# Performance work log

Measured on AMD Instinct MI355X. Metric: run time of the kernel, lower is better.

The kernel has to match this reference:

```python
import jax, jax.numpy as jnp
import numpy as np

EPS = 1e-5

def layer_norm(x, w, b):
    m = jnp.mean(x, axis=-1, keepdims=True)
    v = jnp.mean(jnp.square(x - m), axis=-1, keepdims=True)
    return (x - m) * jax.lax.rsqrt(v + EPS) * w + b

def time_shift(x):
    # shift sequence right by one, zero-pad first step: (B,L,D)
    return jnp.pad(x[:, :-1], ((0, 0), (1, 0), (0, 0)))

def wkv(time_decay, time_first, k, v):
    # Numerically-stable RWKV v4 WKV recurrence. k,v: (B,L,D)
    w = -jnp.exp(time_decay)  # (D,) negative decay
    u = time_first            # (D,)
    B, L, D = k.shape
    kT = jnp.swapaxes(k, 0, 1)  # (L,B,D)
    vT = jnp.swapaxes(v, 0, 1)
    a0 = jnp.zeros((B, D), k.dtype)
    b0 = jnp.zeros((B, D), k.dtype)
    p0 = jnp.full((B, D), -1e38, k.dtype)

    def step(carry, kv_t):
        a, b, p = carry
        k_t, v_t = kv_t
        ww = u + k_t
        q = jnp.maximum(p, ww)
        e1 = jnp.exp(p - q)
        e2 = jnp.exp(ww - q)
        out = (e1 * a + e2 * v_t) / (e1 * b + e2)
        ww2 = p + w
        q2 = jnp.maximum(ww2, k_t)
        e1b = jnp.exp(ww2 - q2)
        e2b = jnp.exp(k_t - q2)
        return (e1b * a + e2b * v_t, e1b * b + e2b, q2), out

    _, outs = jax.lax.scan(step, (a0, b0, p0), (kT, vT))
    return jnp.swapaxes(outs, 0, 1)  # (B,L,D)

def setup_inputs() -> dict:
    key = jax.random.key(0)
    B, L, D, D_att, D_ffn = 8, 2048, 1024, 1024, 4096
    ks = jax.random.split(key, 16)
    s = 1.0 / np.sqrt(D)
    inp = {
        "x": jax.random.normal(ks[0], (B, L, D), jnp.float32),
        "ln_att_w": jnp.ones((D,), jnp.float32),
        "ln_att_b": jnp.zeros((D,), jnp.float32),
        "ln_ffn_w": jnp.ones((D,), jnp.float32),
        "ln_ffn_b": jnp.zeros((D,), jnp.float32),
        "att_time_decay": jax.random.normal(ks[1], (D_att,), jnp.float32) * 0.5,
        "att_time_first": jax.random.normal(ks[2], (D_att,), jnp.float32) * 0.5,
        "att_mix_k": jax.random.uniform(ks[3], (D,), jnp.float32),
        "att_mix_v": jax.random.uniform(ks[4], (D,), jnp.float32),
        "att_mix_r": jax.random.uniform(ks[5], (D,), jnp.float32),
        "att_Wk": jax.random.normal(ks[6], (D_att, D), jnp.float32) * s,
        "att_Wv": jax.random.normal(ks[7], (D_att, D), jnp.float32) * s,
        "att_Wr": jax.random.normal(ks[8], (D_att, D), jnp.float32) * s,
        "att_Wo": jax.random.normal(ks[9], (D, D_att), jnp.float32) * s,
        "ffn_mix_k": jax.random.uniform(ks[10], (D,), jnp.float32),
        "ffn_mix_r": jax.random.uniform(ks[11], (D,), jnp.float32),
        "ffn_Wk": jax.random.normal(ks[12], (D_ffn, D), jnp.float32) * s,
        "ffn_Wv": jax.random.normal(ks[13], (D, D_ffn), jnp.float32) * (1.0 / np.sqrt(D_ffn)),
        "ffn_Wr": jax.random.normal(ks[14], (D, D), jnp.float32) * s,
    }
    return inp

def rwkv_block(x, ln_att_w, ln_att_b, ln_ffn_w, ln_ffn_b,
               att_time_decay, att_time_first, att_mix_k, att_mix_v, att_mix_r,
               att_Wk, att_Wv, att_Wr, att_Wo,
               ffn_mix_k, ffn_mix_r, ffn_Wk, ffn_Wv, ffn_Wr):
    # --- time-mix (WKV attention) ---
    xa = layer_norm(x, ln_att_w, ln_att_b)
    xs = time_shift(xa)
    k = jnp.einsum('bld,ad->bla', xa * att_mix_k + xs * (1.0 - att_mix_k), att_Wk)
    v = jnp.einsum('bld,ad->bla', xa * att_mix_v + xs * (1.0 - att_mix_v), att_Wv)
    r = jnp.einsum('bld,ad->bla', xa * att_mix_r + xs * (1.0 - att_mix_r), att_Wr)
    att = jnp.einsum('bla,da->bld', jax.nn.sigmoid(r) * wkv(att_time_decay, att_time_first, k, v), att_Wo)
    x = x + att
    # --- channel-mix FFN ---
    xf = layer_norm(x, ln_ffn_w, ln_ffn_b)
    xs = time_shift(xf)
    kx = xf * ffn_mix_k + xs * (1.0 - ffn_mix_k)
    rx = xf * ffn_mix_r + xs * (1.0 - ffn_mix_r)
    h = jnp.square(jax.nn.relu(jnp.einsum('bld,fd->blf', kx, ffn_Wk)))
    ffn = jax.nn.sigmoid(jnp.einsum('bld,ed->ble', rx, ffn_Wr)) * jnp.einsum('blf,df->bld', h, ffn_Wv)
    return x + ffn

def reference(x, ln_att_w, ln_att_b, ln_ffn_w, ln_ffn_b,
              att_time_decay, att_time_first, att_mix_k, att_mix_v, att_mix_r,
              att_Wk, att_Wv, att_Wr, att_Wo,
              ffn_mix_k, ffn_mix_r, ffn_Wk, ffn_Wv, ffn_Wr):
    return rwkv_block(x, ln_att_w, ln_att_b, ln_ffn_w, ln_ffn_b,
                      att_time_decay, att_time_first, att_mix_k, att_mix_v, att_mix_r,
                      att_Wk, att_Wv, att_Wr, att_Wo,
                      ffn_mix_k, ffn_mix_r, ffn_Wk, ffn_Wv, ffn_Wr)
```

## Files before the change

### kernel.cpp

```cpp
#include <hip/hip_runtime.h>
#include <stdint.h>

#define DDIM 1024
#define LSEQ 2048
#define BSZ  8
#define FDIM 4096
#define MROWS (BSZ*LSEQ)
#define NCHUNK 32
#define CLEN  (LSEQ/NCHUNK)

typedef float        f32x4  __attribute__((ext_vector_type(4)));
typedef unsigned int u32x4  __attribute__((ext_vector_type(4)));

using gas_void = const __attribute__((address_space(1))) void;
using las_void = __attribute__((address_space(3))) void;

__device__ __forceinline__ void gload16(const void* g, void* l) {
    __builtin_amdgcn_global_load_lds((gas_void*)g, (las_void*)l, 16, 0, 0);
}

__device__ __forceinline__ void mfma_bf16(f32x4& d, u32x4 a, u32x4 b) {
    asm("v_mfma_f32_16x16x32_bf16 %0, %1, %2, %0" : "+v"(d) : "v"(a), "v"(b));
}

__device__ __forceinline__ unsigned short f2bf(float f) {
    __bf16 h = (__bf16)f;
    return __builtin_bit_cast(unsigned short, h);
}

__global__ __launch_bounds__(256) void cvt_bf16(const float* __restrict__ src,
                                                __bf16* __restrict__ dst, int n4)
{
    int i = blockIdx.x * 256 + threadIdx.x;
    if (i >= n4) return;
    float4 f = ((const float4*)src)[i];
    ushort4 o;
    o.x = f2bf(f.x); o.y = f2bf(f.y); o.z = f2bf(f.z); o.w = f2bf(f.w);
    ((ushort4*)dst)[i] = o;
}

__device__ __forceinline__ void blk_reduce4(float& a, float& b, float& c, float& d) {
#pragma unroll
    for (int off = 32; off >= 1; off >>= 1) {
        a += __shfl_xor(a, off, 64);
        b += __shfl_xor(b, off, 64);
        c += __shfl_xor(c, off, 64);
        d += __shfl_xor(d, off, 64);
    }
    __shared__ float sm[4][4];
    const int tid = threadIdx.x;
    if ((tid & 63) == 0) {
        sm[tid >> 6][0] = a; sm[tid >> 6][1] = b;
        sm[tid >> 6][2] = c; sm[tid >> 6][3] = d;
    }
    __syncthreads();
    a = sm[0][0] + sm[1][0] + sm[2][0] + sm[3][0];
    b = sm[0][1] + sm[1][1] + sm[2][1] + sm[3][1];
    c = sm[0][2] + sm[1][2] + sm[2][2] + sm[3][2];
    d = sm[0][3] + sm[1][3] + sm[2][3] + sm[3][3];
}

__global__ __launch_bounds__(256) void ln_mix3(
    const float* __restrict__ xin, const float* __restrict__ lnw, const float* __restrict__ lnb,
    const float* __restrict__ mkv, const float* __restrict__ mvv, const float* __restrict__ mrv,
    __bf16* __restrict__ ok, __bf16* __restrict__ ov, __bf16* __restrict__ orr)
{
    const int row = blockIdx.x;
    const int l   = row & (LSEQ - 1);
    const int tid = threadIdx.x;
    const size_t rbase = (size_t)row * DDIM;
    const float4 cur = ((const float4*)(xin + rbase))[tid];
    float4 prv = make_float4(0.f, 0.f, 0.f, 0.f);
    if (l > 0) prv = ((const float4*)(xin + rbase - DDIM))[tid];
    float s0 = cur.x + cur.y + cur.z + cur.w;
    float q0 = cur.x*cur.x + cur.y*cur.y + cur.z*cur.z + cur.w*cur.w;
    float s1 = prv.x + prv.y + prv.z + prv.w;
    float q1 = prv.x*prv.x + prv.y*prv.y + prv.z*prv.z + prv.w*prv.w;
    blk_reduce4(s0, q0, s1, q1);
    const float inv = 1.f / (float)DDIM;
    const float m0 = s0 * inv, m1 = s1 * inv;
    const float r0 = rsqrtf(fmaxf(q0 * inv - m0*m0, 0.f) + 1e-5f);
    const float r1 = rsqrtf(fmaxf(q1 * inv - m1*m1, 0.f) + 1e-5f);
    const float4 w4 = ((const float4*)lnw)[tid];
    const float4 b4 = ((const float4*)lnb)[tid];
    const float4 k4 = ((const float4*)mkv)[tid];
    const float4 v4 = ((const float4*)mvv)[tid];
    const float4 r4 = ((const float4*)mrv)[tid];
    const float cA[4] = {cur.x, cur.y, cur.z, cur.w};
    const float pA[4] = {prv.x, prv.y, prv.z, prv.w};
    const float wA[4] = {w4.x, w4.y, w4.z, w4.w};
    const float bA[4] = {b4.x, b4.y, b4.z, b4.w};
    const float kA[4] = {k4.x, k4.y, k4.z, k4.w};
    const float vA[4] = {v4.x, v4.y, v4.z, v4.w};
    const float rA[4] = {r4.x, r4.y, r4.z, r4.w};
    ushort4 pk, pv, pr;
    unsigned short* pkp = &pk.x; unsigned short* pvp = &pv.x; unsigned short* prp = &pr.x;
#pragma unroll
    for (int j = 0; j < 4; ++j) {
        float xa = (cA[j] - m0) * r0 * wA[j] + bA[j];
        float xs = (l > 0) ? ((pA[j] - m1) * r1 * wA[j] + bA[j]) : 0.f;
        pkp[j] = f2bf(xa * kA[j] + xs * (1.f - kA[j]));
        pvp[j] = f2bf(xa * vA[j] + xs * (1.f - vA[j]));
        prp[j] = f2bf(xa * rA[j] + xs * (1.f - rA[j]));
    }
    const size_t oi = (size_t)row * (DDIM/4) + tid;
    ((ushort4*)ok)[oi]  = pk;
    ((ushort4*)ov)[oi]  = pv;
    ((ushort4*)orr)[oi] = pr;
}

__global__ __launch_bounds__(256) void ln_mix2(
    const float* __restrict__ xin, const float* __restrict__ lnw, const float* __restrict__ lnb,
    const float* __restrict__ mkv, const float* __restrict__ mrv,
    __bf16* __restrict__ ok, __bf16* __restrict__ orr)
{
    const int row = blockIdx.x;
    const int l   = row & (LSEQ - 1);
    const int tid = threadIdx.x;
    const size_t rbase = (size_t)row * DDIM;
    const float4 cur = ((const float4*)(xin + rbase))[tid];
    float4 prv = make_float4(0.f, 0.f, 0.f, 0.f);
    if (l > 0) prv = ((const float4*)(xin + rbase - DDIM))[tid];
    float s0 = cur.x + cur.y + cur.z + cur.w;
    float q0 = cur.x*cur.x + cur.y*cur.y + cur.z*cur.z + cur.w*cur.w;
    float s1 = prv.x + prv.y + prv.z + prv.w;
    float q1 = prv.x*prv.x + prv.y*prv.y + prv.z*prv.z + prv.w*prv.w;
    blk_reduce4(s0, q0, s1, q1);
    const float inv = 1.f / (float)DDIM;
    const float m0 = s0 * inv, m1 = s1 * inv;
    const float r0 = rsqrtf(fmaxf(q0 * inv - m0*m0, 0.f) + 1e-5f);
    const float r1 = rsqrtf(fmaxf(q1 * inv - m1*m1, 0.f) + 1e-5f);
    const float4 w4 = ((const float4*)lnw)[tid];
    const float4 b4 = ((const float4*)lnb)[tid];
    const float4 k4 = ((const float4*)mkv)[tid];
    const float4 r4 = ((const float4*)mrv)[tid];
    const float cA[4] = {cur.x, cur.y, cur.z, cur.w};
    const float pA[4] = {prv.x, prv.y, prv.z, prv.w};
    const float wA[4] = {w4.x, w4.y, w4.z, w4.w};
    const float bA[4] = {b4.x, b4.y, b4.z, b4.w};
    const float kA[4] = {k4.x, k4.y, k4.z, k4.w};
    const float rA[4] = {r4.x, r4.y, r4.z, r4.w};
    ushort4 pk, pr;
    unsigned short* pkp = &pk.x; unsigned short* prp = &pr.x;
#pragma unroll
    for (int j = 0; j < 4; ++j) {
        float xa = (cA[j] - m0) * r0 * wA[j] + bA[j];
        float xs = (l > 0) ? ((pA[j] - m1) * r1 * wA[j] + bA[j]) : 0.f;
        pkp[j] = f2bf(xa * kA[j] + xs * (1.f - kA[j]));
        prp[j] = f2bf(xa * rA[j] + xs * (1.f - rA[j]));
    }
    const size_t oi = (size_t)row * (DDIM/4) + tid;
    ((ushort4*)ok)[oi]  = pk;
    ((ushort4*)orr)[oi] = pr;
}

__global__ __launch_bounds__(256) void wkv_phase1(
    const __bf16* __restrict__ kin, const __bf16* __restrict__ vin,
    const float* __restrict__ td,
    float* __restrict__ sa, float* __restrict__ sb, float* __restrict__ sp)
{
    const int idx = blockIdx.x * 256 + threadIdx.x;
    const int d  = idx & (DDIM - 1);
    const int bc = idx >> 10;
    const int b  = bc & (BSZ - 1);
    const int c  = bc >> 3;
    const float w = -__expf(td[d]);
    const size_t base = ((size_t)b * LSEQ + (size_t)c * CLEN) * DDIM + d;
    float a = 0.f, bbv = 0.f, p = -1e38f;
    for (int t = 0; t < CLEN; ++t) {
        const size_t off = base + (size_t)t * DDIM;
        const float kt = (float)kin[off];
        const float vt = (float)vin[off];
        const float ww2 = p + w;
        const float q2  = fmaxf(ww2, kt);
        const float e1  = __expf(ww2 - q2);
        const float e2  = __expf(kt - q2);
        a   = e1 * a   + e2 * vt;
        bbv = e1 * bbv + e2;
        p   = q2;
    }
    sa[idx] = a; sb[idx] = bbv; sp[idx] = p;
}

__global__ __launch_bounds__(256) void wkv_phase2(
    const __bf16* __restrict__ kin, const __bf16* __restrict__ vin,
    const __bf16* __restrict__ srin,
    const float* __restrict__ td, const float* __restrict__ tf,
    const float* __restrict__ sa, const float* __restrict__ sb,
    const float* __restrict__ sp,
    __bf16* __restrict__ outp)
{
    const int idx = blockIdx.x * 256 + threadIdx.x;
    const int d  = idx & (DDIM - 1);
    const int bc = idx >> 10;
    const int b  = bc & (BSZ - 1);
    const int c  = bc >> 3;
    const float w = -__expf(td[d]);
    const float u = tf[d];
    const float nw = (float)CLEN * w;

    float a = 0.f, bbv = 0.f, p = -1e38f;
    for (int j = 0; j < c; ++j) {
        const int sidx = ((j * BSZ + b) << 10) + d;
        const float aj = sa[sidx], bj = sb[sidx], pj = sp[sidx];
        const float ps = p + nw;
        const float pn = fmaxf(ps, pj);
        const float e1 = __expf(ps - pn);
        const float e2 = __expf(pj - pn);
        a   = e1 * a   + e2 * aj;
        bbv = e1 * bbv + e2 * bj;
        p   = pn;
    }

    const size_t base = ((size_t)b * LSEQ + (size_t)c * CLEN) * DDIM + d;
    for (int t = 0; t < CLEN; ++t) {
        const size_t off = base + (size_t)t * DDIM;
        const float kt = (float)kin[off];
        const float vt = (float)vin[off];
        const float sr = (float)srin[off];
        const float ww = u + kt;
        const float q  = fmaxf(p, ww);
        const float e1 = __expf(p - q);
        const float e2 = __expf(ww - q);
        const float o  = (e1 * a + e2 * vt) / (e1 * bbv + e2);
        outp[off] = (__bf16)(sr * o);
        const float ww2 = p + w;
        const float q2  = fmaxf(ww2, kt);
        const float e1b = __expf(ww2 - q2);
        const float e2b = __expf(kt - q2);
        a   = e1b * a   + e2b * vt;
        bbv = e1b * bbv + e2b;
        p   = q2;
    }
}

template<int EPI>
__global__ __launch_bounds__(512, 2)
void gemm8(const __bf16* __restrict__ A, const __bf16* __restrict__ Bw,
           float* outF, __bf16* outH,
           const float* auxF, const __bf16* __restrict__ auxH,
           int N, int K, int gy)
{
    __shared__ __align__(16) char smem[131072];
    const int tid  = threadIdx.x;
    const int lane = tid & 63;
    const int wid  = tid >> 6;
    const int wr = wid >> 2, wc = wid & 3;

    const int nwg = gridDim.x;
    const int f = blockIdx.x;
    const int g = (f & 7) * (nwg >> 3) + (f >> 3);
    const int tx = g / gy;
    const int ty = g - tx * gy;
    const size_t row0 = (size_t)tx * 256;
    const size_t col0 = (size_t)ty * 256;

    auto stage = [&](int buf, int k0, int isB, int q) {
        const int row  = q * 128 + (tid >> 2);
        const int slot = (tid & 3) ^ ((row >> 1) & 3);
        const __bf16* gp = (isB ? Bw + (col0 + row) * (size_t)K
                                : A  + (row0 + row) * (size_t)K) + k0 + slot * 8;
        char* lp = smem + buf * 32768 + isB * 16384 + q * 8192 + wid * 1024;
        gload16(gp, lp);
    };
    auto rdA = [&](int buf, int m) -> u32x4 {
        const int row  = wr * 128 + m * 16 + (lane & 15);
        const int slot = (lane >> 4) ^ ((row >> 1) & 3);
        return *(const u32x4*)(smem + buf * 32768 + row * 64 + slot * 16);
    };
    auto rdB = [&](int buf, int n) -> u32x4 {
        const int row  = wc * 64 + n * 16 + (lane & 15);
        const int slot = (lane >> 4) ^ ((row >> 1) & 3);
        return *(const u32x4*)(smem + buf * 32768 + 16384 + row * 64 + slot * 16);
    };

    f32x4 acc[8][4] = {};
    const int ns = K / 32;

    stage(0, 0, 0, 0); stage(0, 0, 0, 1); stage(0, 0, 1, 0); stage(0, 0, 1, 1);
    stage(1, 32, 0, 0); stage(1, 32, 0, 1); stage(1, 32, 1, 0); stage(1, 32, 1, 1);

    for (int t = 0; t < ns; ++t) {
        const int cb = t & 3;
        if (t < ns - 1) asm volatile("s_waitcnt vmcnt(4)" ::: "memory");
        else            asm volatile("s_waitcnt vmcnt(0)" ::: "memory");
        __builtin_amdgcn_s_barrier();

        const int pf = t + 2;
        const int pb = pf & 3;
        const int pk = pf * 32;

        u32x4 bfr[4];
#pragma unroll
        for (int n = 0; n < 4; ++n) bfr[n] = rdB(cb, n);
        u32x4 afr[4];
#pragma unroll
        for (int m = 0; m < 4; ++m) afr[m] = rdA(cb, m);
        if (pf < ns) { stage(pb, pk, 0, 0); stage(pb, pk, 0, 1); }
        __builtin_amdgcn_s_setprio(1);
#pragma unroll
        for (int m = 0; m < 4; ++m)
#pragma unroll
            for (int n = 0; n < 4; ++n)
                mfma_bf16(acc[m][n], afr[m], bfr[n]);
        __builtin_amdgcn_s_setprio(0);
        __builtin_amdgcn_s_barrier();

#pragma unroll
        for (int m = 0; m < 4; ++m) afr[m] = rdA(cb, m + 4);
        if (pf < ns) { stage(pb, pk, 1, 0); stage(pb, pk, 1, 1); }
        __builtin_amdgcn_s_setprio(1);
#pragma unroll
        for (int m = 0; m < 4; ++m)
#pragma unroll
            for (int n = 0; n < 4; ++n)
                mfma_bf16(acc[m + 4][n], afr[m], bfr[n]);
        __builtin_amdgcn_s_setprio(0);
    }
    asm volatile("s_nop 7\n\ts_nop 7\n\ts_nop 3");

    const size_t obr = row0 + wr * 128 + ((lane >> 4) << 2);
    const size_t obc = col0 + wc * 64 + (lane & 15);
#pragma unroll
    for (int m = 0; m < 8; ++m) {
#pragma unroll
        for (int n = 0; n < 4; ++n) {
#pragma unroll
            for (int j = 0; j < 4; ++j) {
                const size_t idx = (obr + m * 16 + j) * (size_t)N + obc + n * 16;
                const float v = acc[m][n][j];
                if constexpr (EPI == 1) {
                    outH[idx] = (__bf16)(1.f / (1.f + __expf(-v)));
                } else if constexpr (EPI == 2) {
                    const float t2 = fmaxf(v, 0.f);
                    outH[idx] = (__bf16)(t2 * t2);
                } else if constexpr (EPI == 3) {
                    outF[idx] = auxF[idx] + v;
                } else if constexpr (EPI == 4) {
                    outF[idx] = auxF[idx] + (float)auxH[idx] * v;
                } else {
                    outH[idx] = (__bf16)v;
                }
            }
        }
    }
}

extern "C" void kernel_launch(void* const* d_in, const int* in_sizes, int n_in,
                              void* d_out, int out_size, void* d_ws, size_t ws_size,
                              hipStream_t stream)
{
    const float* x    = (const float*)d_in[0];
    const float* lnaw = (const float*)d_in[1];
    const float* lnab = (const float*)d_in[2];
    const float* lnfw = (const float*)d_in[3];
    const float* lnfb = (const float*)d_in[4];
    const float* tdec = (const float*)d_in[5];
    const float* tfir = (const float*)d_in[6];
    const float* amk  = (const float*)d_in[7];
    const float* amv  = (const float*)d_in[8];
    const float* amr  = (const float*)d_in[9];
    const float* aWk  = (const float*)d_in[10];
    const float* aWv  = (const float*)d_in[11];
    const float* aWr  = (const float*)d_in[12];
    const float* aWo  = (const float*)d_in[13];
    const float* fmk  = (const float*)d_in[14];
    const float* fmr  = (const float*)d_in[15];
    const float* fWk  = (const float*)d_in[16];
    const float* fWv  = (const float*)d_in[17];
    const float* fWr  = (const float*)d_in[18];
    float* out = (float*)d_out;

    char* ws = (char*)d_ws;
    const size_t MiB = 1ull << 20;
    __bf16* Wk_h  = (__bf16*)ws;
    __bf16* Wv_h  = Wk_h + (1ull << 20);
    __bf16* Wr_h  = Wk_h + (2ull << 20);
    __bf16* Wo_h  = Wk_h + (3ull << 20);
    __bf16* fWk_h = Wk_h + (4ull << 20);
    __bf16* fWv_h = Wk_h + (8ull << 20);
    __bf16* fWr_h = Wk_h + (12ull << 20);
    __bf16* xk = (__bf16*)(ws + 26 * MiB);
    __bf16* xv = (__bf16*)(ws + 58 * MiB);
    __bf16* xr = (__bf16*)(ws + 90 * MiB);
    __bf16* kb = (__bf16*)(ws + 122 * MiB);
    __bf16* vb = (__bf16*)(ws + 154 * MiB);
    __bf16* sr = (__bf16*)(ws + 186 * MiB);
    float* st_a = (float*)(ws + 218 * MiB);
    float* st_b = (float*)(ws + 219 * MiB);
    float* st_p = (float*)(ws + 220 * MiB);
    __bf16* atta = xk;
    __bf16* kx   = xv;
    __bf16* rx   = xr;
    __bf16* sb   = xk;
    __bf16* hb   = (__bf16*)(ws + 90 * MiB);

    cvt_bf16<<<1024, 256, 0, stream>>>(aWk, Wk_h,  1 << 18);
    cvt_bf16<<<1024, 256, 0, stream>>>(aWv, Wv_h,  1 << 18);
    cvt_bf16<<<1024, 256, 0, stream>>>(aWr, Wr_h,  1 << 18);
    cvt_bf16<<<1024, 256, 0, stream>>>(aWo, Wo_h,  1 << 18);
    cvt_bf16<<<4096, 256, 0, stream>>>(fWk, fWk_h, 1 << 20);
    cvt_bf16<<<4096, 256, 0, stream>>>(fWv, fWv_h, 1 << 20);
    cvt_bf16<<<1024, 256, 0, stream>>>(fWr, fWr_h, 1 << 18);

    ln_mix3<<<MROWS, 256, 0, stream>>>(x, lnaw, lnab, amk, amv, amr, xk, xv, xr);

    const int gD = (MROWS / 256) * (DDIM / 256);
    const int gF = (MROWS / 256) * (FDIM / 256);
    gemm8<5><<<gD, 512, 0, stream>>>(xk, Wk_h, nullptr, kb, nullptr, nullptr, DDIM, DDIM, DDIM/256);
    gemm8<5><<<gD, 512, 0, stream>>>(xv, Wv_h, nullptr, vb, nullptr, nullptr, DDIM, DDIM, DDIM/256);
    gemm8<1><<<gD, 512, 0, stream>>>(xr, Wr_h, nullptr, sr, nullptr, nullptr, DDIM, DDIM, DDIM/256);

    const int nthreads = BSZ * DDIM * NCHUNK;
    wkv_phase1<<<nthreads / 256, 256, 0, stream>>>(kb, vb, tdec, st_a, st_b, st_p);
    wkv_phase2<<<nthreads / 256, 256, 0, stream>>>(kb, vb, sr, tdec, tfir,
                                                   st_a, st_b, st_p, atta);

    gemm8<3><<<gD, 512, 0, stream>>>(atta, Wo_h, out, nullptr, x, nullptr, DDIM, DDIM, DDIM/256);

    ln_mix2<<<MROWS, 256, 0, stream>>>(out, lnfw, lnfb, fmk, fmr, kx, rx);

    gemm8<1><<<gD, 512, 0, stream>>>(rx, fWr_h, nullptr, sb, nullptr, nullptr, DDIM, DDIM, DDIM/256);

    gemm8<2><<<gF, 512, 0, stream>>>(kx, fWk_h, nullptr, hb, nullptr, nullptr, FDIM, DDIM, FDIM/256);

    gemm8<4><<<gD, 512, 0, stream>>>(hb, fWv_h, out, nullptr, out, sb, DDIM, FDIM, DDIM/256);
}
```

Baseline: 737.4 us.

## Deepen GEMM prefetch to three stages and merge weight conversion launches

The GEMM main loop now prefetches three k-steps ahead instead of two, using all four LDS buffers, and adjusts the vmcnt waits to match. The mid-iteration barrier is removed and a separate register array is used for the second half of A fragments. Separately, the seven bf16 weight-conversion kernels are merged into one launch that finds its segment through a cumulative-offset table. Together these aim to hide more global-load latency and cut launch overhead, at the risk of an LDS buffer race now that the mid-iteration barrier is gone and the prefetch distance is deeper.

```diff
diff --git a/kernel.cpp b/kernel.cpp
--- a/kernel.cpp
+++ b/kernel.cpp
@@ -28,15 +28,24 @@
     return __builtin_bit_cast(unsigned short, h);
 }
 
-__global__ __launch_bounds__(256) void cvt_bf16(const float* __restrict__ src,
-                                                __bf16* __restrict__ dst, int n4)
-{
-    int i = blockIdx.x * 256 + threadIdx.x;
-    if (i >= n4) return;
-    float4 f = ((const float4*)src)[i];
+struct CvtArgs {
+    const float* s[7];
+    __bf16*      d[7];
+    int          cum[8];
+};
+
+__global__ __launch_bounds__(256) void cvt_all(CvtArgs a)
+{
+    const int i = blockIdx.x * 256 + threadIdx.x;
+    if (i >= a.cum[7]) return;
+    int seg = 0;
+#pragma unroll 6
+    while (i >= a.cum[seg + 1]) ++seg;
+    const int off = i - a.cum[seg];
+    float4 f = ((const float4*)a.s[seg])[off];
     ushort4 o;
     o.x = f2bf(f.x); o.y = f2bf(f.y); o.z = f2bf(f.z); o.w = f2bf(f.w);
-    ((ushort4*)dst)[i] = o;
+    ((ushort4*)a.d[seg])[off] = o;
 }
 
 __device__ __forceinline__ void blk_reduce4(float& a, float& b, float& c, float& d) {
@@ -277,16 +286,18 @@
     f32x4 acc[8][4] = {};
     const int ns = K / 32;
 
-    stage(0, 0, 0, 0); stage(0, 0, 0, 1); stage(0, 0, 1, 0); stage(0, 0, 1, 1);
+    stage(0,  0, 0, 0); stage(0,  0, 0, 1); stage(0,  0, 1, 0); stage(0,  0, 1, 1);
     stage(1, 32, 0, 0); stage(1, 32, 0, 1); stage(1, 32, 1, 0); stage(1, 32, 1, 1);
+    stage(2, 64, 0, 0); stage(2, 64, 0, 1); stage(2, 64, 1, 0); stage(2, 64, 1, 1);
 
     for (int t = 0; t < ns; ++t) {
         const int cb = t & 3;
-        if (t < ns - 1) asm volatile("s_waitcnt vmcnt(4)" ::: "memory");
-        else            asm volatile("s_waitcnt vmcnt(0)" ::: "memory");
+        if (t < ns - 2)       asm volatile("s_waitcnt vmcnt(8)" ::: "memory");
+        else if (t == ns - 2) asm volatile("s_waitcnt vmcnt(4)" ::: "memory");
+        else                  asm volatile("s_waitcnt vmcnt(0)" ::: "memory");
         __builtin_amdgcn_s_barrier();
 
-        const int pf = t + 2;
+        const int pf = t + 3;
         const int pb = pf & 3;
         const int pk = pf * 32;
 
@@ -304,17 +315,17 @@
             for (int n = 0; n < 4; ++n)
                 mfma_bf16(acc[m][n], afr[m], bfr[n]);
         __builtin_amdgcn_s_setprio(0);
-        __builtin_amdgcn_s_barrier();
-
-#pragma unroll
-        for (int m = 0; m < 4; ++m) afr[m] = rdA(cb, m + 4);
+
+        u32x4 afr2[4];
+#pragma unroll
+        for (int m = 0; m < 4; ++m) afr2[m] = rdA(cb, m + 4);
         if (pf < ns) { stage(pb, pk, 1, 0); stage(pb, pk, 1, 1); }
         __builtin_amdgcn_s_setprio(1);
 #pragma unroll
         for (int m = 0; m < 4; ++m)
 #pragma unroll
             for (int n = 0; n < 4; ++n)
-                mfma_bf16(acc[m + 4][n], afr[m], bfr[n]);
+                mfma_bf16(acc[m + 4][n], afr2[m], bfr[n]);
         __builtin_amdgcn_s_setprio(0);
     }
     asm volatile("s_nop 7\n\ts_nop 7\n\ts_nop 3");
@@ -395,13 +406,21 @@
     __bf16* sb   = xk;
     __bf16* hb   = (__bf16*)(ws + 90 * MiB);
 
-    cvt_bf16<<<1024, 256, 0, stream>>>(aWk, Wk_h,  1 << 18);
-    cvt_bf16<<<1024, 256, 0, stream>>>(aWv, Wv_h,  1 << 18);
-    cvt_bf16<<<1024, 256, 0, stream>>>(aWr, Wr_h,  1 << 18);
-    cvt_bf16<<<1024, 256, 0, stream>>>(aWo, Wo_h,  1 << 18);
-    cvt_bf16<<<4096, 256, 0, stream>>>(fWk, fWk_h, 1 << 20);
-    cvt_bf16<<<4096, 256, 0, stream>>>(fWv, fWv_h, 1 << 20);
-    cvt_bf16<<<1024, 256, 0, stream>>>(fWr, fWr_h, 1 << 18);
+    CvtArgs ca;
+    ca.s[0] = aWk;  ca.d[0] = Wk_h;
+    ca.s[1] = aWv;  ca.d[1] = Wv_h;
+    ca.s[2] = aWr;  ca.d[2] = Wr_h;
+    ca.s[3] = aWo;  ca.d[3] = Wo_h;
+    ca.s[4] = fWk;  ca.d[4] = fWk_h;
+    ca.s[5] = fWv;  ca.d[5] = fWv_h;
+    ca.s[6] = fWr;  ca.d[6] = fWr_h;
+    {
+        const int sz[7] = {1<<18, 1<<18, 1<<18, 1<<18, 1<<20, 1<<20, 1<<18};
+        int c = 0;
+        for (int i = 0; i < 7; ++i) { ca.cum[i] = c; c += sz[i]; }
+        ca.cum[7] = c;
+    }
+    cvt_all<<<(ca.cum[7] + 255) / 256, 256, 0, stream>>>(ca);
 
     ln_mix3<<<MROWS, 256, 0, stream>>>(x, lnaw, lnab, amk, amv, amr, xk, xv, xr);
 
```

New measurement: 719.4 us. 2.4% less time.
